# Kernel tuning notes

Hardware: AMD Instinct MI355X
Metric: run time of the kernel (lower is better)

Reference implementation:

```python
import jax, jax.numpy as jnp
import numpy as np

LEAK = 0.1
EPS = 1e-5

N, C, T, V = 32, 64, 400, 27
S, IC, O = 2, 16, 64  # num_subset, inter_channels, out_channels


def _make_pe(channel, joint_num, time_len):
    pos = np.tile(np.arange(joint_num), time_len).astype(np.float32)[:, None]
    div = np.exp(np.arange(0, channel, 2).astype(np.float32) * (-(np.log(10000.0) / channel)))
    pe = np.zeros((time_len * joint_num, channel), np.float32)
    pe[:, 0::2] = np.sin(pos * div)
    pe[:, 1::2] = np.cos(pos * div)
    # (T*V, C) -> (1, C, T, V)
    return jnp.asarray(pe.reshape(time_len, joint_num, channel).transpose(2, 0, 1)[None])


def setup_inputs() -> dict:
    key = jax.random.key(0)
    ks = jax.random.split(key, 16)
    w = lambda k, shp, fan: jax.random.normal(k, shp, jnp.float32) * (1.0 / np.sqrt(fan))
    inp = {
        "x": jax.random.normal(ks[0], (N, C, T, V), jnp.float32),
        "pe": _make_pe(C, V, T),
        # in_nets: Conv2d(C, 2*S*IC, 1)
        "W_in": w(ks[1], (2 * S * IC, C), C),
        "b_in": jnp.zeros((2 * S * IC,), jnp.float32),
        "alphas": jnp.ones((1, S, 1, 1), jnp.float32),
        "att0": jnp.ones((1, S, V, V), jnp.float32) / V,
        # out_nets: Conv2d(S*C, O, 1) + BN
        "W_out": w(ks[2], (O, S * C), S * C),
        "b_out": jnp.zeros((O,), jnp.float32),
        "g_out": jnp.ones((O,), jnp.float32),
        "be_out": jnp.zeros((O,), jnp.float32),
        "m_out": jax.random.normal(ks[3], (O,), jnp.float32) * 0.1,
        "v_out": jax.random.uniform(ks[4], (O,), jnp.float32, 0.5, 1.5),
        # ff_nets: Conv2d(O, O, 1) + BN
        "W_ff": w(ks[5], (O, O), O),
        "b_ff": jnp.zeros((O,), jnp.float32),
        "g_ff": jnp.ones((O,), jnp.float32),
        "be_ff": jnp.zeros((O,), jnp.float32),
        "m_ff": jax.random.normal(ks[6], (O,), jnp.float32) * 0.1,
        "v_ff": jax.random.uniform(ks[7], (O,), jnp.float32, 0.5, 1.5),
        # out_nett: Conv2d(O, O, (3,1), pad (1,0)) + BN
        "W_t": w(ks[8], (O, O, 3, 1), O * 3),
        "b_t": jnp.zeros((O,), jnp.float32),
        "g_t": jnp.ones((O,), jnp.float32),
        "be_t": jnp.zeros((O,), jnp.float32),
        "m_t": jax.random.normal(ks[9], (O,), jnp.float32) * 0.1,
        "v_t": jax.random.uniform(ks[10], (O,), jnp.float32, 0.5, 1.5),
    }
    return inp


def _lrelu(x):
    return jnp.where(x >= 0, x, LEAK * x)


def _bn(x, g, b, m, v):
    scale = g / jnp.sqrt(v + EPS)
    return (x - m[None, :, None, None]) * scale[None, :, None, None] + b[None, :, None, None]


def _conv1x1(x, W, b):
    return jnp.einsum('oc,nctv->notv', W, x) + b[None, :, None, None]


def reference(x, pe, W_in, b_in, alphas, att0, W_out, b_out, g_out, be_out, m_out, v_out,
              W_ff, b_ff, g_ff, be_ff, m_ff, v_ff, W_t, b_t, g_t, be_t, m_t, v_t):
    n, c, t, v_ = x.shape
    s = alphas.shape[1]
    ic = W_in.shape[0] // (2 * s)
    # positional encoding on the attention-input branch only
    y = x + pe[:, :, :t]
    qk = _conv1x1(y, W_in, b_in).reshape(n, 2 * s, ic, t, v_)
    q, k = qk[:, :s], qk[:, s:]
    # atts buffer is zeros; dropout is identity in eval
    att = jnp.tanh(jnp.einsum('nsctu,nsctv->nsuv', q, k) / (ic * t)) * alphas + att0
    y = jnp.einsum('nctu,nsuv->nsctv', x, att).reshape(n, s * c, t, v_)
    y = _bn(_conv1x1(y, W_out, b_out), g_out, be_out, m_out, v_out)
    y = _lrelu(x + y)  # downs1 = identity
    yf = _bn(_conv1x1(y, W_ff, b_ff), g_ff, be_ff, m_ff, v_ff)
    y = _lrelu(x + yf)  # downs2 = identity
    z = jax.lax.conv_general_dilated(
        y, W_t, window_strides=(1, 1), padding=((1, 1), (0, 0)),
        dimension_numbers=('NCHW', 'OIHW', 'NCHW'))
    z = _bn(z + b_t[None, :, None, None], g_t, be_t, m_t, v_t)
    z = _lrelu(y + z)  # downt2 = identity
    return z
```

## Files before the change

kernel.cpp:

```cpp
#include <hip/hip_runtime.h>
#include <hip/hip_bf16.h>

typedef __hip_bfloat16 bf16;
typedef unsigned short u16;
typedef __attribute__((ext_vector_type(8))) short short8;
typedef __attribute__((ext_vector_type(4))) short s4v;
typedef __attribute__((ext_vector_type(4))) float f32x4;

#define LEAK 0.1f
#define EPS_ 1e-5f
#define MFMA(a, b, c) __builtin_amdgcn_mfma_f32_16x16x32_bf16(a, b, c, 0, 0, 0)

__device__ __forceinline__ float u2f(u16 u) { return __uint_as_float(((unsigned int)u) << 16); }
__device__ __forceinline__ u16 f2u(float f) {
  bf16 h = __float2bfloat16(f);
  u16 r;
  __builtin_memcpy(&r, &h, 2);
  return r;
}
__device__ __forceinline__ f32x4 z4() { f32x4 z = {0.f, 0.f, 0.f, 0.f}; return z; }

__global__ __launch_bounds__(256) void k_att_mfma(
    const float* __restrict__ x, const float* __restrict__ pe,
    const float* __restrict__ W_in, const float* __restrict__ b_in,
    float* __restrict__ att)
{
  __shared__ __align__(16) u16 syT[2][32][72];
  __shared__ __align__(16) u16 sqkT[2][32][72];
  const int tid = threadIdx.x;
  const int w = tid >> 6, lane = tid & 63;
  const int m = lane & 15, quad = lane >> 4;
  const int n = blockIdx.y, t0 = blockIdx.x * 16;
  const int s_w = w >> 1, mtu = w & 1;

  for (int i = tid; i < 2 * 32 * 72; i += 256) { syT[0][0][i] = 0; sqkT[0][0][i] = 0; }

  short8 aW[2];
#pragma unroll
  for (int kf = 0; kf < 2; ++kf) {
    short8 tt;
#pragma unroll
    for (int j = 0; j < 8; ++j)
      tt[j] = (short)f2u(W_in[(16 * w + m) * 64 + 32 * kf + 8 * quad + j]);
    aW[kf] = tt;
  }
  float bb[4];
#pragma unroll
  for (int r = 0; r < 4; ++r) bb[r] = b_in[16 * w + quad * 4 + r];
  f32x4 accA0 = z4(), accA1 = z4();
  __syncthreads();

  for (int it = 0; it < 8; ++it) {
    const int t = t0 + 2 * it;
    for (int i = tid; i < 64 * 54; i += 256) {
      int c = i / 54, r = i % 54;
      int sl = r / 27, v = r % 27;
      syT[sl][v][c] = f2u(x[((n * 64 + c) * 400 + t) * 27 + r] +
                          pe[(c * 400 + t) * 27 + r]);
    }
    __syncthreads();
#pragma unroll
    for (int sl = 0; sl < 2; ++sl) {
      f32x4 a0 = z4(), a1 = z4();
#pragma unroll
      for (int kf = 0; kf < 2; ++kf) {
        short8 b0 = *(const short8*)&syT[sl][m][32 * kf + 8 * quad];
        short8 b1 = *(const short8*)&syT[sl][16 + m][32 * kf + 8 * quad];
        a0 = MFMA(aW[kf], b0, a0);
        a1 = MFMA(aW[kf], b1, a1);
      }
#pragma unroll
      for (int nt = 0; nt < 2; ++nt) {
        f32x4 a = nt ? a1 : a0;
        int v = 16 * nt + m;
        if (v < 27) {
          s4v pk;
#pragma unroll
          for (int reg = 0; reg < 4; ++reg) pk[reg] = (short)f2u(a[reg] + bb[reg]);
          *(s4v*)&sqkT[sl][v][16 * w + quad * 4] = pk;
        }
      }
    }
    __syncthreads();
    {
      short8 aQ  = *(const short8*)&sqkT[quad >> 1][16 * mtu + m][16 * s_w + 8 * (quad & 1)];
      short8 bK0 = *(const short8*)&sqkT[quad >> 1][m][32 + 16 * s_w + 8 * (quad & 1)];
      short8 bK1 = *(const short8*)&sqkT[quad >> 1][16 + m][32 + 16 * s_w + 8 * (quad & 1)];
      accA0 = MFMA(aQ, bK0, accA0);
      accA1 = MFMA(aQ, bK1, accA1);
    }
    __syncthreads();
  }
#pragma unroll
  for (int nt = 0; nt < 2; ++nt) {
    f32x4 a = nt ? accA1 : accA0;
#pragma unroll
    for (int reg = 0; reg < 4; ++reg) {
      int u = 16 * mtu + quad * 4 + reg, v = 16 * nt + m;
      if (u < 27 && v < 27)
        atomicAdd(&att[(n * 2 + s_w) * 729 + u * 27 + v], a[reg]);
    }
  }
}

__global__ __launch_bounds__(256) void k_att_fin(
    float* __restrict__ att, const float* __restrict__ alphas,
    const float* __restrict__ att0)
{
  int i = blockIdx.x * 256 + threadIdx.x;
  if (i >= 32 * 2 * 729) return;
  int s = (i / 729) & 1;
  int r = i % 729;
  att[i] = tanhf(att[i] * (1.f / 6400.f)) * alphas[s] + att0[s * 729 + r];
}

__global__ __launch_bounds__(256) void k_fused_mfma(
    const float* __restrict__ x, const float* __restrict__ att,
    const float* __restrict__ W_out, const float* __restrict__ b_out,
    const float* __restrict__ g_out, const float* __restrict__ be_out,
    const float* __restrict__ m_out, const float* __restrict__ v_out,
    const float* __restrict__ W_ff, const float* __restrict__ b_ff,
    const float* __restrict__ g_ff, const float* __restrict__ be_ff,
    const float* __restrict__ m_ff, const float* __restrict__ v_ff,
    const float* __restrict__ W_t, const float* __restrict__ b_t,
    const float* __restrict__ g_t, const float* __restrict__ be_t,
    const float* __restrict__ m_t, const float* __restrict__ v_t,
    float* __restrict__ out)
{
  __shared__ __align__(16) u16 sx[2][64][40];
  __shared__ __align__(16) u16 sy2[2][32][136];
  __shared__ __align__(16) u16 sy3[2][32][72];
  __shared__ __align__(16) u16 sy4[4][32][72];
  const int tid = threadIdx.x;
  const int w = tid >> 6, lane = tid & 63;
  const int m = lane & 15, quad = lane >> 4;
  const int n = blockIdx.y, t0 = blockIdx.x * 8;

  for (int i = tid; i < 2 * 64 * 40; i += 256) sx[0][0][i] = 0;
  for (int i = tid; i < 2 * 32 * 136; i += 256) sy2[0][0][i] = 0;
  for (int i = tid; i < 2 * 32 * 72; i += 256) sy3[0][0][i] = 0;
  for (int i = tid; i < 4 * 32 * 72; i += 256) sy4[0][0][i] = 0;

  short8 aWo[4], aWf[2], aWt[6], bAtt[4];
#pragma unroll
  for (int kf = 0; kf < 4; ++kf) {
    short8 tt;
#pragma unroll
    for (int j = 0; j < 8; ++j)
      tt[j] = (short)f2u(W_out[(16 * w + m) * 128 + 32 * kf + 8 * quad + j]);
    aWo[kf] = tt;
  }
#pragma unroll
  for (int kf = 0; kf < 2; ++kf) {
    short8 tt;
#pragma unroll
    for (int j = 0; j < 8; ++j)
      tt[j] = (short)f2u(W_ff[(16 * w + m) * 64 + 32 * kf + 8 * quad + j]);
    aWf[kf] = tt;
  }
#pragma unroll
  for (int kf = 0; kf < 6; ++kf) {
    short8 tt;
    int dt = kf >> 1;
#pragma unroll
    for (int j = 0; j < 8; ++j) {
      int ii = 32 * (kf & 1) + 8 * quad + j;
      tt[j] = (short)f2u(W_t[((16 * w + m) * 64 + ii) * 3 + dt]);
    }
    aWt[kf] = tt;
  }
#pragma unroll
  for (int s = 0; s < 2; ++s)
#pragma unroll
    for (int nt = 0; nt < 2; ++nt) {
      short8 tt;
#pragma unroll
      for (int j = 0; j < 8; ++j) {
        int u = 8 * quad + j, v = 16 * nt + m;
        tt[j] = (u < 27 && v < 27) ? (short)f2u(att[(n * 2 + s) * 729 + u * 27 + v]) : (short)0;
      }
      bAtt[s * 2 + nt] = tt;
    }
  float Ao[4], Bo[4], Af[4], Bf[4], At[4], Bt[4];
#pragma unroll
  for (int reg = 0; reg < 4; ++reg) {
    int o = 16 * w + quad * 4 + reg;
    float sc;
    sc = g_out[o] * rsqrtf(v_out[o] + EPS_); Ao[reg] = sc; Bo[reg] = (b_out[o] - m_out[o]) * sc + be_out[o];
    sc = g_ff[o] * rsqrtf(v_ff[o] + EPS_);   Af[reg] = sc; Bf[reg] = (b_ff[o] - m_ff[o]) * sc + be_ff[o];
    sc = g_t[o] * rsqrtf(v_t[o] + EPS_);     At[reg] = sc; Bt[reg] = (b_t[o] - m_t[o]) * sc + be_t[o];
  }
  __syncthreads();

  for (int p = 0; p < 5; ++p) {
    const int tA = t0 - 1 + 2 * p;
    const bool val0 = (tA >= 0) && (tA < 400);
    const bool val1 = (tA + 1 >= 0) && (tA + 1 < 400);
    if (val0 && val1) {
      for (int i = tid; i < 64 * 54; i += 256) {
        int c = i / 54, r = i % 54;
        sx[r / 27][c][r % 27] = f2u(x[((n * 64 + c) * 400 + tA) * 27 + r]);
      }
    } else {
#pragma unroll
      for (int sl = 0; sl < 2; ++sl) {
        if (!(sl ? val1 : val0)) continue;
        int t = tA + sl;
        for (int i = tid; i < 1728; i += 256) {
          int c = i / 27, u = i % 27;
          sx[sl][c][u] = f2u(x[((n * 64 + c) * 400 + t) * 27 + u]);
        }
      }
    }
    __syncthreads();
#pragma unroll
    for (int sl = 0; sl < 2; ++sl) {
      if (!(sl ? val1 : val0)) continue;
      short8 ax = *(const short8*)&sx[sl][16 * w + m][8 * quad];
      f32x4 acc[4];
#pragma unroll
      for (int f = 0; f < 4; ++f) acc[f] = MFMA(ax, bAtt[f], z4());
#pragma unroll
      for (int s = 0; s < 2; ++s)
#pragma unroll
        for (int nt = 0; nt < 2; ++nt) {
          int v = 16 * nt + m;
          if (v < 27) {
            f32x4 a = acc[s * 2 + nt];
            s4v pk;
#pragma unroll
            for (int reg = 0; reg < 4; ++reg) pk[reg] = (short)f2u(a[reg]);
            *(s4v*)&sy2[sl][v][s * 64 + 16 * w + quad * 4] = pk;
          }
        }
    }
    __syncthreads();
#pragma unroll
    for (int sl = 0; sl < 2; ++sl) {
      if (!(sl ? val1 : val0)) continue;
      f32x4 a0 = z4(), a1 = z4();
#pragma unroll
      for (int kf = 0; kf < 4; ++kf) {
        short8 b0 = *(const short8*)&sy2[sl][m][32 * kf + 8 * quad];
        short8 b1 = *(const short8*)&sy2[sl][16 + m][32 * kf + 8 * quad];
        a0 = MFMA(aWo[kf], b0, a0);
        a1 = MFMA(aWo[kf], b1, a1);
      }
#pragma unroll
      for (int nt = 0; nt < 2; ++nt) {
        f32x4 a = nt ? a1 : a0;
        int v = 16 * nt + m;
        if (v < 27) {
          s4v pk;
#pragma unroll
          for (int reg = 0; reg < 4; ++reg) {
            int o = 16 * w + quad * 4 + reg;
            float r = u2f(sx[sl][o][v]) + a[reg] * Ao[reg] + Bo[reg];
            pk[reg] = (short)f2u((r >= 0.f) ? r : LEAK * r);
          }
          *(s4v*)&sy3[sl][v][16 * w + quad * 4] = pk;
        }
      }
    }
    __syncthreads();
#pragma unroll
    for (int sl = 0; sl < 2; ++sl) {
      int st = 2 * p + sl;
      int slot = st & 3;
      if (sl ? val1 : val0) {
        f32x4 a0 = z4(), a1 = z4();
#pragma unroll
        for (int kf = 0; kf < 2; ++kf) {
          short8 b0 = *(const short8*)&sy3[sl][m][32 * kf + 8 * quad];
          short8 b1 = *(const short8*)&sy3[sl][16 + m][32 * kf + 8 * quad];
          a0 = MFMA(aWf[kf], b0, a0);
          a1 = MFMA(aWf[kf], b1, a1);
        }
#pragma unroll
        for (int nt = 0; nt < 2; ++nt) {
          f32x4 a = nt ? a1 : a0;
          int v = 16 * nt + m;
          if (v < 27) {
            s4v pk;
#pragma unroll
            for (int reg = 0; reg < 4; ++reg) {
              int o = 16 * w + quad * 4 + reg;
              float r = u2f(sx[sl][o][v]) + a[reg] * Af[reg] + Bf[reg];
              pk[reg] = (short)f2u((r >= 0.f) ? r : LEAK * r);
            }
            *(s4v*)&sy4[slot][v][16 * w + quad * 4] = pk;
          }
        }
      } else {
        s4v zz = {0, 0, 0, 0};
        for (int i = tid; i < 576; i += 256)
          ((s4v*)&sy4[slot][0][0])[i] = zz;
      }
    }
    __syncthreads();
    if (p >= 1) {
#pragma unroll
      for (int cc = 0; cc < 2; ++cc) {
        int st_c = 2 * p - 1 + cc;
        int t_out = t0 + st_c - 1;
        f32x4 a0 = z4(), a1 = z4();
#pragma unroll
        for (int kf = 0; kf < 6; ++kf) {
          int slot = (st_c - 1 + (kf >> 1)) & 3;
          int col = 32 * (kf & 1) + 8 * quad;
          short8 b0 = *(const short8*)&sy4[slot][m][col];
          short8 b1 = *(const short8*)&sy4[slot][16 + m][col];
          a0 = MFMA(aWt[kf], b0, a0);
          a1 = MFMA(aWt[kf], b1, a1);
        }
#pragma unroll
        for (int nt = 0; nt < 2; ++nt) {
          f32x4 a = nt ? a1 : a0;
          int v = 16 * nt + m;
          if (v < 27) {
#pragma unroll
            for (int reg = 0; reg < 4; ++reg) {
              int o = 16 * w + quad * 4 + reg;
              float r = u2f(sy4[st_c & 3][v][o]) + a[reg] * At[reg] + Bt[reg];
              out[((n * 64 + o) * 400 + t_out) * 27 + v] = (r >= 0.f) ? r : LEAK * r;
            }
          }
        }
      }
    }
  }
}

extern "C" void kernel_launch(void* const* d_in, const int* in_sizes, int n_in,
                              void* d_out, int out_size, void* d_ws, size_t ws_size,
                              hipStream_t stream)
{
  const float* x      = (const float*)d_in[0];
  const float* pe     = (const float*)d_in[1];
  const float* W_in   = (const float*)d_in[2];
  const float* b_in   = (const float*)d_in[3];
  const float* alphas = (const float*)d_in[4];
  const float* att0   = (const float*)d_in[5];
  const float* W_out  = (const float*)d_in[6];
  const float* b_out  = (const float*)d_in[7];
  const float* g_out  = (const float*)d_in[8];
  const float* be_out = (const float*)d_in[9];
  const float* m_out  = (const float*)d_in[10];
  const float* v_out  = (const float*)d_in[11];
  const float* W_ff   = (const float*)d_in[12];
  const float* b_ff   = (const float*)d_in[13];
  const float* g_ff   = (const float*)d_in[14];
  const float* be_ff  = (const float*)d_in[15];
  const float* m_ff   = (const float*)d_in[16];
  const float* v_ff   = (const float*)d_in[17];
  const float* W_t    = (const float*)d_in[18];
  const float* b_t    = (const float*)d_in[19];
  const float* g_t    = (const float*)d_in[20];
  const float* be_t   = (const float*)d_in[21];
  const float* m_t    = (const float*)d_in[22];
  const float* v_t    = (const float*)d_in[23];

  float* att = (float*)d_ws;

  hipMemsetAsync(att, 0, 32 * 2 * 729 * sizeof(float), stream);
  k_att_mfma<<<dim3(25, 32), 256, 0, stream>>>(x, pe, W_in, b_in, att);
  k_att_fin<<<dim3((32 * 2 * 729 + 255) / 256), 256, 0, stream>>>(att, alphas, att0);
  k_fused_mfma<<<dim3(50, 32), 256, 0, stream>>>(
      x, att,
      W_out, b_out, g_out, be_out, m_out, v_out,
      W_ff, b_ff, g_ff, be_ff, m_ff, v_ff,
      W_t, b_t, g_t, be_t, m_t, v_t,
      (float*)d_out);
}
```

Measured before the change: 434.4 us.

## Split pipeline into four kernels with bf16 q/k and y3 staged in global memory

Replaces the attention kernel with two kernels. The first computes q and k as bf16 and stores them to the workspace in a u-major layout. The second performs the full T-length reduction per (n, s) without atomics, then applies tanh, alpha and att0, which removes the memset and the separate finalize kernel. The fused tail is split into g_ab (attention apply, out-conv, BN, residual) writing a bf16 channel-last y3 buffer, and g_cd (ff conv and temporal conv), which recomputes halo timesteps instead of streaming them. This adds global round trips for q/k and y3 and gives the attention reduction only 64 blocks, trading that for simpler per-block work and fewer barriers.

```diff
diff --git a/kernel.cpp b/kernel.cpp
--- a/kernel.cpp
+++ b/kernel.cpp
@@ -6,6 +6,7 @@
 typedef __attribute__((ext_vector_type(8))) short short8;
 typedef __attribute__((ext_vector_type(4))) short s4v;
 typedef __attribute__((ext_vector_type(4))) float f32x4;
+typedef __attribute__((ext_vector_type(4))) unsigned int u32x4;
 
 #define LEAK 0.1f
 #define EPS_ 1e-5f
@@ -20,20 +21,16 @@
 }
 __device__ __forceinline__ f32x4 z4() { f32x4 z = {0.f, 0.f, 0.f, 0.f}; return z; }
 
-__global__ __launch_bounds__(256) void k_att_mfma(
+__global__ __launch_bounds__(256) void g_qk(
     const float* __restrict__ x, const float* __restrict__ pe,
     const float* __restrict__ W_in, const float* __restrict__ b_in,
-    float* __restrict__ att)
-{
-  __shared__ __align__(16) u16 syT[2][32][72];
-  __shared__ __align__(16) u16 sqkT[2][32][72];
+    u16* __restrict__ qG, u16* __restrict__ kG)
+{
+  __shared__ u32x4 sB[16][2][64];
   const int tid = threadIdx.x;
   const int w = tid >> 6, lane = tid & 63;
   const int m = lane & 15, quad = lane >> 4;
-  const int n = blockIdx.y, t0 = blockIdx.x * 16;
-  const int s_w = w >> 1, mtu = w & 1;
-
-  for (int i = tid; i < 2 * 32 * 72; i += 256) { syT[0][0][i] = 0; sqkT[0][0][i] = 0; }
+  const int n = blockIdx.y, p0 = blockIdx.x * 256;
 
   short8 aW[2];
 #pragma unroll
@@ -47,78 +44,195 @@
   float bb[4];
 #pragma unroll
   for (int r = 0; r < 4; ++r) bb[r] = b_in[16 * w + quad * 4 + r];
-  f32x4 accA0 = z4(), accA1 = z4();
+
+#pragma unroll
+  for (int k = 0; k < 8; ++k) {
+    int slot = tid + 256 * k;
+    int tile = slot >> 7, kf = (slot >> 6) & 1;
+    int qq = (slot >> 4) & 3, mm = slot & 15;
+    int p = p0 + tile * 16 + mm;
+    int c0 = kf * 32 + qq * 8;
+    short8 tt = {0, 0, 0, 0, 0, 0, 0, 0};
+    if (p < 10800) {
+#pragma unroll
+      for (int j = 0; j < 8; ++j)
+        tt[j] = (short)f2u(x[(n * 64 + c0 + j) * 10800 + p] +
+                           pe[(c0 + j) * 10800 + p]);
+    }
+    *(short8*)&sB[tile][kf][slot & 63] = tt;
+  }
   __syncthreads();
 
-  for (int it = 0; it < 8; ++it) {
-    const int t = t0 + 2 * it;
-    for (int i = tid; i < 64 * 54; i += 256) {
-      int c = i / 54, r = i % 54;
-      int sl = r / 27, v = r % 27;
-      syT[sl][v][c] = f2u(x[((n * 64 + c) * 400 + t) * 27 + r] +
-                          pe[(c * 400 + t) * 27 + r]);
-    }
-    __syncthreads();
-#pragma unroll
-    for (int sl = 0; sl < 2; ++sl) {
-      f32x4 a0 = z4(), a1 = z4();
-#pragma unroll
-      for (int kf = 0; kf < 2; ++kf) {
-        short8 b0 = *(const short8*)&syT[sl][m][32 * kf + 8 * quad];
-        short8 b1 = *(const short8*)&syT[sl][16 + m][32 * kf + 8 * quad];
-        a0 = MFMA(aW[kf], b0, a0);
-        a1 = MFMA(aW[kf], b1, a1);
-      }
-#pragma unroll
-      for (int nt = 0; nt < 2; ++nt) {
-        f32x4 a = nt ? a1 : a0;
-        int v = 16 * nt + m;
-        if (v < 27) {
-          s4v pk;
-#pragma unroll
-          for (int reg = 0; reg < 4; ++reg) pk[reg] = (short)f2u(a[reg] + bb[reg]);
-          *(s4v*)&sqkT[sl][v][16 * w + quad * 4] = pk;
-        }
-      }
-    }
-    __syncthreads();
-    {
-      short8 aQ  = *(const short8*)&sqkT[quad >> 1][16 * mtu + m][16 * s_w + 8 * (quad & 1)];
-      short8 bK0 = *(const short8*)&sqkT[quad >> 1][m][32 + 16 * s_w + 8 * (quad & 1)];
-      short8 bK1 = *(const short8*)&sqkT[quad >> 1][16 + m][32 + 16 * s_w + 8 * (quad & 1)];
-      accA0 = MFMA(aQ, bK0, accA0);
-      accA1 = MFMA(aQ, bK1, accA1);
-    }
-    __syncthreads();
-  }
-#pragma unroll
-  for (int nt = 0; nt < 2; ++nt) {
-    f32x4 a = nt ? accA1 : accA0;
-#pragma unroll
-    for (int reg = 0; reg < 4; ++reg) {
-      int u = 16 * mtu + quad * 4 + reg, v = 16 * nt + m;
-      if (u < 27 && v < 27)
-        atomicAdd(&att[(n * 2 + s_w) * 729 + u * 27 + v], a[reg]);
-    }
-  }
-}
-
-__global__ __launch_bounds__(256) void k_att_fin(
-    float* __restrict__ att, const float* __restrict__ alphas,
-    const float* __restrict__ att0)
-{
-  int i = blockIdx.x * 256 + threadIdx.x;
-  if (i >= 32 * 2 * 729) return;
-  int s = (i / 729) & 1;
-  int r = i % 729;
-  att[i] = tanhf(att[i] * (1.f / 6400.f)) * alphas[s] + att0[s * 729 + r];
-}
-
-__global__ __launch_bounds__(256) void k_fused_mfma(
+  u16* dst = (w < 2 ? qG : kG) + (n * 2 + (w & 1)) * 32 * 6400;
+#pragma unroll 4
+  for (int tile = 0; tile < 16; ++tile) {
+    short8 b0 = *(const short8*)&sB[tile][0][lane];
+    short8 b1 = *(const short8*)&sB[tile][1][lane];
+    f32x4 acc = MFMA(aW[0], b0, z4());
+    acc = MFMA(aW[1], b1, acc);
+    int p = p0 + tile * 16 + m;
+    if (p < 10800) {
+      unsigned t = (unsigned)p / 27u;
+      unsigned u = (unsigned)p - 27u * t;
+      s4v pk;
+#pragma unroll
+      for (int reg = 0; reg < 4; ++reg) pk[reg] = (short)f2u(acc[reg] + bb[reg]);
+      *(s4v*)&dst[(u * 400 + t) * 16 + quad * 4] = pk;
+    }
+  }
+}
+
+__global__ __launch_bounds__(256) void g_att(
+    const u16* __restrict__ qG, const u16* __restrict__ kG,
+    const float* __restrict__ alphas, const float* __restrict__ att0,
+    float* __restrict__ att)
+{
+  __shared__ float sred[4][64][16];
+  const int tid = threadIdx.x;
+  const int w = tid >> 6, lane = tid & 63;
+  const int m = lane & 15, quad = lane >> 4;
+  const int s = blockIdx.x, n = blockIdx.y;
+  const u16* qb = qG + (n * 2 + s) * 32 * 6400;
+  const u16* kb = kG + (n * 2 + s) * 32 * 6400;
+
+  f32x4 a00 = z4(), a01 = z4(), a10 = z4(), a11 = z4();
+#pragma unroll 2
+  for (int it = 0; it < 25; ++it) {
+    int kk0 = w * 1600 + it * 64;
+#pragma unroll
+    for (int kf = 0; kf < 2; ++kf) {
+      int kk = kk0 + kf * 32 + quad * 8;
+      short8 aq0 = *(const short8*)&qb[m * 6400 + kk];
+      short8 aq1 = *(const short8*)&qb[(16 + m) * 6400 + kk];
+      short8 bk0 = *(const short8*)&kb[m * 6400 + kk];
+      short8 bk1 = *(const short8*)&kb[(16 + m) * 6400 + kk];
+      a00 = MFMA(aq0, bk0, a00);
+      a01 = MFMA(aq0, bk1, a01);
+      a10 = MFMA(aq1, bk0, a10);
+      a11 = MFMA(aq1, bk1, a11);
+    }
+  }
+  *(f32x4*)&sred[w][lane][0] = a00;
+  *(f32x4*)&sred[w][lane][4] = a01;
+  *(f32x4*)&sred[w][lane][8] = a10;
+  *(f32x4*)&sred[w][lane][12] = a11;
+  __syncthreads();
+  const float al = alphas[s];
+#pragma unroll
+  for (int k = 0; k < 4; ++k) {
+    int slot = tid + 256 * k;
+    int lsrc = slot >> 4, idx = slot & 15;
+    float val = sred[0][lsrc][idx] + sred[1][lsrc][idx] +
+                sred[2][lsrc][idx] + sred[3][lsrc][idx];
+    int f = idx >> 2, reg = idx & 3;
+    int ut = f >> 1, vt = f & 1;
+    int qq = lsrc >> 4, mm = lsrc & 15;
+    int u = ut * 16 + qq * 4 + reg, v = vt * 16 + mm;
+    if (u < 27 && v < 27)
+      att[(n * 2 + s) * 729 + u * 27 + v] =
+          tanhf(val * (1.f / 6400.f)) * al + att0[s * 729 + u * 27 + v];
+  }
+}
+
+__global__ __launch_bounds__(256) void g_ab(
     const float* __restrict__ x, const float* __restrict__ att,
     const float* __restrict__ W_out, const float* __restrict__ b_out,
     const float* __restrict__ g_out, const float* __restrict__ be_out,
     const float* __restrict__ m_out, const float* __restrict__ v_out,
+    u16* __restrict__ y3T)
+{
+  __shared__ u32x4 sy2f[4][2][4][64];
+  const int tid = threadIdx.x;
+  const int w = tid >> 6, lane = tid & 63;
+  const int m = lane & 15, quad = lane >> 4;
+  const int n = blockIdx.y, t0 = blockIdx.x * 4;
+
+  short8 bAtt[4];
+#pragma unroll
+  for (int s = 0; s < 2; ++s)
+#pragma unroll
+    for (int nt = 0; nt < 2; ++nt) {
+      short8 tt;
+#pragma unroll
+      for (int j = 0; j < 8; ++j) {
+        int u = 8 * quad + j, v = 16 * nt + m;
+        tt[j] = (u < 27 && v < 27) ? (short)f2u(att[(n * 2 + s) * 729 + u * 27 + v]) : (short)0;
+      }
+      bAtt[s * 2 + nt] = tt;
+    }
+  short8 aWo[4];
+#pragma unroll
+  for (int kf = 0; kf < 4; ++kf) {
+    short8 tt;
+#pragma unroll
+    for (int j = 0; j < 8; ++j)
+      tt[j] = (short)f2u(W_out[(16 * w + m) * 128 + 32 * kf + 8 * quad + j]);
+    aWo[kf] = tt;
+  }
+  float Ao[4], Bo[4];
+#pragma unroll
+  for (int reg = 0; reg < 4; ++reg) {
+    int o = 16 * w + quad * 4 + reg;
+    float sc = g_out[o] * rsqrtf(v_out[o] + EPS_);
+    Ao[reg] = sc;
+    Bo[reg] = (b_out[o] - m_out[o]) * sc + be_out[o];
+  }
+
+  const int q1 = quad & 1;
+  const int qp = (2 * w + (quad >> 1)) & 3;
+#pragma unroll
+  for (int tc = 0; tc < 4; ++tc) {
+    int t = t0 + tc;
+    short8 ax;
+#pragma unroll
+    for (int j = 0; j < 8; ++j) {
+      int u = quad * 8 + j;
+      ax[j] = (u < 27) ? (short)f2u(x[((n * 64 + 16 * w + m) * 400 + t) * 27 + u]) : (short)0;
+    }
+    f32x4 acc[4];
+#pragma unroll
+    for (int f = 0; f < 4; ++f) acc[f] = MFMA(ax, bAtt[f], z4());
+#pragma unroll
+    for (int s = 0; s < 2; ++s)
+#pragma unroll
+      for (int nt = 0; nt < 2; ++nt) {
+        f32x4 a = acc[s * 2 + nt];
+        s4v pk;
+#pragma unroll
+        for (int reg = 0; reg < 4; ++reg) pk[reg] = (short)f2u(a[reg]);
+        int kfp = 2 * s + (w >> 1);
+        *(s4v*)((u16*)&sy2f[tc][nt][kfp][qp * 16 + m] + 4 * q1) = pk;
+      }
+  }
+  __syncthreads();
+#pragma unroll
+  for (int tc = 0; tc < 4; ++tc) {
+    int t = t0 + tc;
+#pragma unroll
+    for (int vt = 0; vt < 2; ++vt) {
+      f32x4 a0 = z4();
+#pragma unroll
+      for (int kf = 0; kf < 4; ++kf) {
+        short8 b = *(const short8*)&sy2f[tc][vt][kf][lane];
+        a0 = MFMA(aWo[kf], b, a0);
+      }
+      int v = vt * 16 + m;
+      if (v < 27) {
+        s4v pk;
+#pragma unroll
+        for (int reg = 0; reg < 4; ++reg) {
+          int o = 16 * w + quad * 4 + reg;
+          float r = x[((n * 64 + o) * 400 + t) * 27 + v] + a0[reg] * Ao[reg] + Bo[reg];
+          pk[reg] = (short)f2u((r >= 0.f) ? r : LEAK * r);
+        }
+        *(s4v*)&y3T[(unsigned)(n * 10800 + t * 27 + v) * 64 + 16 * w + quad * 4] = pk;
+      }
+    }
+  }
+}
+
+__global__ __launch_bounds__(256) void g_cd(
+    const float* __restrict__ x, const u16* __restrict__ y3T,
     const float* __restrict__ W_ff, const float* __restrict__ b_ff,
     const float* __restrict__ g_ff, const float* __restrict__ be_ff,
     const float* __restrict__ m_ff, const float* __restrict__ v_ff,
@@ -127,29 +241,13 @@
     const float* __restrict__ m_t, const float* __restrict__ v_t,
     float* __restrict__ out)
 {
-  __shared__ __align__(16) u16 sx[2][64][40];
-  __shared__ __align__(16) u16 sy2[2][32][136];
-  __shared__ __align__(16) u16 sy3[2][32][72];
-  __shared__ __align__(16) u16 sy4[4][32][72];
+  __shared__ u32x4 sy4f[6][2][2][64];
   const int tid = threadIdx.x;
   const int w = tid >> 6, lane = tid & 63;
   const int m = lane & 15, quad = lane >> 4;
-  const int n = blockIdx.y, t0 = blockIdx.x * 8;
-
-  for (int i = tid; i < 2 * 64 * 40; i += 256) sx[0][0][i] = 0;
-  for (int i = tid; i < 2 * 32 * 136; i += 256) sy2[0][0][i] = 0;
-  for (int i = tid; i < 2 * 32 * 72; i += 256) sy3[0][0][i] = 0;
-  for (int i = tid; i < 4 * 32 * 72; i += 256) sy4[0][0][i] = 0;
-
-  short8 aWo[4], aWf[2], aWt[6], bAtt[4];
-#pragma unroll
-  for (int kf = 0; kf < 4; ++kf) {
-    short8 tt;
-#pragma unroll
-    for (int j = 0; j < 8; ++j)
-      tt[j] = (short)f2u(W_out[(16 * w + m) * 128 + 32 * kf + 8 * quad + j]);
-    aWo[kf] = tt;
-  }
+  const int n = blockIdx.y, t0 = blockIdx.x * 4;
+
+  short8 aWf[2], aWt[6];
 #pragma unroll
   for (int kf = 0; kf < 2; ++kf) {
     short8 tt;
@@ -169,162 +267,75 @@
     }
     aWt[kf] = tt;
   }
-#pragma unroll
-  for (int s = 0; s < 2; ++s)
-#pragma unroll
-    for (int nt = 0; nt < 2; ++nt) {
-      short8 tt;
-#pragma unroll
-      for (int j = 0; j < 8; ++j) {
-        int u = 8 * quad + j, v = 16 * nt + m;
-        tt[j] = (u < 27 && v < 27) ? (short)f2u(att[(n * 2 + s) * 729 + u * 27 + v]) : (short)0;
-      }
-      bAtt[s * 2 + nt] = tt;
-    }
-  float Ao[4], Bo[4], Af[4], Bf[4], At[4], Bt[4];
+  float Af[4], Bf[4], At[4], Bt[4];
 #pragma unroll
   for (int reg = 0; reg < 4; ++reg) {
     int o = 16 * w + quad * 4 + reg;
     float sc;
-    sc = g_out[o] * rsqrtf(v_out[o] + EPS_); Ao[reg] = sc; Bo[reg] = (b_out[o] - m_out[o]) * sc + be_out[o];
-    sc = g_ff[o] * rsqrtf(v_ff[o] + EPS_);   Af[reg] = sc; Bf[reg] = (b_ff[o] - m_ff[o]) * sc + be_ff[o];
-    sc = g_t[o] * rsqrtf(v_t[o] + EPS_);     At[reg] = sc; Bt[reg] = (b_t[o] - m_t[o]) * sc + be_t[o];
+    sc = g_ff[o] * rsqrtf(v_ff[o] + EPS_); Af[reg] = sc; Bf[reg] = (b_ff[o] - m_ff[o]) * sc + be_ff[o];
+    sc = g_t[o] * rsqrtf(v_t[o] + EPS_);   At[reg] = sc; Bt[reg] = (b_t[o] - m_t[o]) * sc + be_t[o];
+  }
+
+  const int q1 = quad & 1;
+  const int qp = (2 * w + (quad >> 1)) & 3;
+  const int kfp = w >> 1;
+  f32x4 y4res[4][2];
+#pragma unroll
+  for (int tl = 0; tl < 6; ++tl) {
+    int t = t0 - 1 + tl;
+    if (t >= 0 && t < 400) {
+#pragma unroll
+      for (int vt = 0; vt < 2; ++vt) {
+        int v = vt * 16 + m;
+        unsigned p = (unsigned)(n * 10800 + t * 27 + v);
+        f32x4 acc = z4();
+#pragma unroll
+        for (int kf = 0; kf < 2; ++kf) {
+          short8 b = *(const short8*)&y3T[p * 64 + kf * 32 + quad * 8];
+          acc = MFMA(aWf[kf], b, acc);
+        }
+        s4v pk;
+        f32x4 yr;
+#pragma unroll
+        for (int reg = 0; reg < 4; ++reg) {
+          int o = 16 * w + quad * 4 + reg;
+          float xr = (v < 27) ? x[((n * 64 + o) * 400 + t) * 27 + v] : 0.f;
+          float r = xr + acc[reg] * Af[reg] + Bf[reg];
+          r = (r >= 0.f) ? r : LEAK * r;
+          yr[reg] = r;
+          pk[reg] = (short)f2u(r);
+        }
+        if (tl >= 1 && tl <= 4) y4res[tl - 1][vt] = yr;
+        *(s4v*)((u16*)&sy4f[tl][vt][kfp][qp * 16 + m] + 4 * q1) = pk;
+      }
+    } else {
+      s4v zz = {0, 0, 0, 0};
+#pragma unroll
+      for (int vt = 0; vt < 2; ++vt) {
+        if (tl >= 1 && tl <= 4) y4res[tl - 1][vt] = z4();
+        *(s4v*)((u16*)&sy4f[tl][vt][kfp][qp * 16 + m] + 4 * q1) = zz;
+      }
+    }
   }
   __syncthreads();
-
-  for (int p = 0; p < 5; ++p) {
-    const int tA = t0 - 1 + 2 * p;
-    const bool val0 = (tA >= 0) && (tA < 400);
-    const bool val1 = (tA + 1 >= 0) && (tA + 1 < 400);
-    if (val0 && val1) {
-      for (int i = tid; i < 64 * 54; i += 256) {
-        int c = i / 54, r = i % 54;
-        sx[r / 27][c][r % 27] = f2u(x[((n * 64 + c) * 400 + tA) * 27 + r]);
-      }
-    } else {
-#pragma unroll
-      for (int sl = 0; sl < 2; ++sl) {
-        if (!(sl ? val1 : val0)) continue;
-        int t = tA + sl;
-        for (int i = tid; i < 1728; i += 256) {
-          int c = i / 27, u = i % 27;
-          sx[sl][c][u] = f2u(x[((n * 64 + c) * 400 + t) * 27 + u]);
-        }
-      }
-    }
-    __syncthreads();
-#pragma unroll
-    for (int sl = 0; sl < 2; ++sl) {
-      if (!(sl ? val1 : val0)) continue;
-      short8 ax = *(const short8*)&sx[sl][16 * w + m][8 * quad];
-      f32x4 acc[4];
-#pragma unroll
-      for (int f = 0; f < 4; ++f) acc[f] = MFMA(ax, bAtt[f], z4());
-#pragma unroll
-      for (int s = 0; s < 2; ++s)
-#pragma unroll
-        for (int nt = 0; nt < 2; ++nt) {
-          int v = 16 * nt + m;
-          if (v < 27) {
-            f32x4 a = acc[s * 2 + nt];
-            s4v pk;
-#pragma unroll
-            for (int reg = 0; reg < 4; ++reg) pk[reg] = (short)f2u(a[reg]);
-            *(s4v*)&sy2[sl][v][s * 64 + 16 * w + quad * 4] = pk;
-          }
-        }
-    }
-    __syncthreads();
-#pragma unroll
-    for (int sl = 0; sl < 2; ++sl) {
-      if (!(sl ? val1 : val0)) continue;
-      f32x4 a0 = z4(), a1 = z4();
-#pragma unroll
-      for (int kf = 0; kf < 4; ++kf) {
-        short8 b0 = *(const short8*)&sy2[sl][m][32 * kf + 8 * quad];
-        short8 b1 = *(const short8*)&sy2[sl][16 + m][32 * kf + 8 * quad];
-        a0 = MFMA(aWo[kf], b0, a0);
-        a1 = MFMA(aWo[kf], b1, a1);
-      }
-#pragma unroll
-      for (int nt = 0; nt < 2; ++nt) {
-        f32x4 a = nt ? a1 : a0;
-        int v = 16 * nt + m;
-        if (v < 27) {
-          s4v pk;
-#pragma unroll
-          for (int reg = 0; reg < 4; ++reg) {
-            int o = 16 * w + quad * 4 + reg;
-            float r = u2f(sx[sl][o][v]) + a[reg] * Ao[reg] + Bo[reg];
-            pk[reg] = (short)f2u((r >= 0.f) ? r : LEAK * r);
-          }
-          *(s4v*)&sy3[sl][v][16 * w + quad * 4] = pk;
-        }
-      }
-    }
-    __syncthreads();
-#pragma unroll
-    for (int sl = 0; sl < 2; ++sl) {
-      int st = 2 * p + sl;
-      int slot = st & 3;
-      if (sl ? val1 : val0) {
-        f32x4 a0 = z4(), a1 = z4();
-#pragma unroll
-        for (int kf = 0; kf < 2; ++kf) {
-          short8 b0 = *(const short8*)&sy3[sl][m][32 * kf + 8 * quad];
-          short8 b1 = *(const short8*)&sy3[sl][16 + m][32 * kf + 8 * quad];
-          a0 = MFMA(aWf[kf], b0, a0);
-          a1 = MFMA(aWf[kf], b1, a1);
-        }
-#pragma unroll
-        for (int nt = 0; nt < 2; ++nt) {
-          f32x4 a = nt ? a1 : a0;
-          int v = 16 * nt + m;
-          if (v < 27) {
-            s4v pk;
-#pragma unroll
-            for (int reg = 0; reg < 4; ++reg) {
-              int o = 16 * w + quad * 4 + reg;
-              float r = u2f(sx[sl][o][v]) + a[reg] * Af[reg] + Bf[reg];
-              pk[reg] = (short)f2u((r >= 0.f) ? r : LEAK * r);
-            }
-            *(s4v*)&sy4[slot][v][16 * w + quad * 4] = pk;
-          }
-        }
-      } else {
-        s4v zz = {0, 0, 0, 0};
-        for (int i = tid; i < 576; i += 256)
-          ((s4v*)&sy4[slot][0][0])[i] = zz;
-      }
-    }
-    __syncthreads();
-    if (p >= 1) {
-#pragma unroll
-      for (int cc = 0; cc < 2; ++cc) {
-        int st_c = 2 * p - 1 + cc;
-        int t_out = t0 + st_c - 1;
-        f32x4 a0 = z4(), a1 = z4();
-#pragma unroll
-        for (int kf = 0; kf < 6; ++kf) {
-          int slot = (st_c - 1 + (kf >> 1)) & 3;
-          int col = 32 * (kf & 1) + 8 * quad;
-          short8 b0 = *(const short8*)&sy4[slot][m][col];
-          short8 b1 = *(const short8*)&sy4[slot][16 + m][col];
-          a0 = MFMA(aWt[kf], b0, a0);
-          a1 = MFMA(aWt[kf], b1, a1);
-        }
-#pragma unroll
-        for (int nt = 0; nt < 2; ++nt) {
-          f32x4 a = nt ? a1 : a0;
-          int v = 16 * nt + m;
-          if (v < 27) {
-#pragma unroll
-            for (int reg = 0; reg < 4; ++reg) {
-              int o = 16 * w + quad * 4 + reg;
-              float r = u2f(sy4[st_c & 3][v][o]) + a[reg] * At[reg] + Bt[reg];
-              out[((n * 64 + o) * 400 + t_out) * 27 + v] = (r >= 0.f) ? r : LEAK * r;
-            }
-          }
+#pragma unroll
+  for (int tc = 0; tc < 4; ++tc) {
+    int t = t0 + tc;
+#pragma unroll
+    for (int vt = 0; vt < 2; ++vt) {
+      f32x4 acc = z4();
+#pragma unroll
+      for (int kf = 0; kf < 6; ++kf) {
+        short8 b = *(const short8*)&sy4f[tc + (kf >> 1)][vt][kf & 1][lane];
+        acc = MFMA(aWt[kf], b, acc);
+      }
+      int v = vt * 16 + m;
+      if (v < 27) {
+#pragma unroll
+        for (int reg = 0; reg < 4; ++reg) {
+          int o = 16 * w + quad * 4 + reg;
+          float r = y4res[tc][vt][reg] + acc[reg] * At[reg] + Bt[reg];
+          out[((n * 64 + o) * 400 + t) * 27 + v] = (r >= 0.f) ? r : LEAK * r;
         }
       }
     }
@@ -361,14 +372,15 @@
   const float* v_t    = (const float*)d_in[23];
 
   float* att = (float*)d_ws;
-
-  hipMemsetAsync(att, 0, 32 * 2 * 729 * sizeof(float), stream);
-  k_att_mfma<<<dim3(25, 32), 256, 0, stream>>>(x, pe, W_in, b_in, att);
-  k_att_fin<<<dim3((32 * 2 * 729 + 255) / 256), 256, 0, stream>>>(att, alphas, att0);
-  k_fused_mfma<<<dim3(50, 32), 256, 0, stream>>>(
-      x, att,
-      W_out, b_out, g_out, be_out, m_out, v_out,
-      W_ff, b_ff, g_ff, be_ff, m_ff, v_ff,
-      W_t, b_t, g_t, be_t, m_t, v_t,
-      (float*)d_out);
-}
+  u16* qG  = (u16*)((char*)d_ws + (1u << 20));
+  u16* kG  = (u16*)((char*)d_ws + (1u << 20) + 26214400u);
+  u16* y3T = (u16*)((char*)d_ws + (1u << 20));
+
+  g_qk<<<dim3(43, 32), 256, 0, stream>>>(x, pe, W_in, b_in, qG, kG);
+  g_att<<<dim3(2, 32), 256, 0, stream>>>(qG, kG, alphas, att0, att);
+  g_ab<<<dim3(100, 32), 256, 0, stream>>>(
+      x, att, W_out, b_out, g_out, be_out, m_out, v_out, y3T);
+  g_cd<<<dim3(100, 32), 256, 0, stream>>>(
+      x, y3T, W_ff, b_ff, g_ff, be_ff, m_ff, v_ff,
+      W_t, b_t, g_t, be_t, m_t, v_t, (float*)d_out);
+}
```

New measurement: 462.6 us. 1.07x slower.
